# Kernel tuning notes

Hardware: AMD Instinct MI355X
Metric: run time of the kernel (lower is better)

Reference implementation:

```python
import jax, jax.numpy as jnp
import numpy as np

H = 3  # hidden size (matches nn.LSTM(3, 3, ...))


def _lstm_dir(x, Wih, Whh, bih, bhh, reverse):
    """One direction of one LSTM layer. x: [B,T,D]; PyTorch gate order i,f,g,o."""
    B = x.shape[0]
    xT = jnp.swapaxes(x, 0, 1)  # [T,B,D]
    # Precompute input projection for all timesteps (memory-bound GEMM once).
    x_proj = jnp.einsum('tbd,gd->tbg', xT, Wih) + (bih + bhh)  # [T,B,4H]

    def step(carry, xp):
        h, c = carry
        gates = xp + h @ Whh.T  # [B,4H]
        i = jax.nn.sigmoid(gates[:, :H])
        f = jax.nn.sigmoid(gates[:, H:2 * H])
        g = jnp.tanh(gates[:, 2 * H:3 * H])
        o = jax.nn.sigmoid(gates[:, 3 * H:])
        c = f * c + i * g
        h = o * jnp.tanh(c)
        return (h, c), h

    init = (jnp.zeros((B, H), x.dtype), jnp.zeros((B, H), x.dtype))
    _, hs = jax.lax.scan(step, init, x_proj, reverse=reverse)
    return jnp.swapaxes(hs, 0, 1)  # [B,T,H], time-aligned with input


def setup_inputs() -> dict:
    key = jax.random.key(0)
    ks = jax.random.split(key, 20)
    B, T = 8192, 512
    k = 1.0 / np.sqrt(H)

    def u(kk, shape):
        return jax.random.uniform(kk, shape, jnp.float32, -k, k)

    inp = {"x": jax.random.normal(ks[0], (B, T, 3), jnp.float32)}
    # layer 0: input dim 3; layer 1: input dim 2*H = 6
    inp.update({
        "W_ih_l0": u(ks[1], (4 * H, 3)),  "W_hh_l0": u(ks[2], (4 * H, H)),
        "b_ih_l0": u(ks[3], (4 * H,)),    "b_hh_l0": u(ks[4], (4 * H,)),
        "W_ih_l0r": u(ks[5], (4 * H, 3)), "W_hh_l0r": u(ks[6], (4 * H, H)),
        "b_ih_l0r": u(ks[7], (4 * H,)),   "b_hh_l0r": u(ks[8], (4 * H,)),
        "W_ih_l1": u(ks[9], (4 * H, 2 * H)),  "W_hh_l1": u(ks[10], (4 * H, H)),
        "b_ih_l1": u(ks[11], (4 * H,)),       "b_hh_l1": u(ks[12], (4 * H,)),
        "W_ih_l1r": u(ks[13], (4 * H, 2 * H)),"W_hh_l1r": u(ks[14], (4 * H, H)),
        "b_ih_l1r": u(ks[15], (4 * H,)),      "b_hh_l1r": u(ks[16], (4 * H,)),
        "W_lin": u(ks[17], (1, 2 * H)),       "b_lin": u(ks[18], (1,)),
    })
    return inp


def reference(x, W_ih_l0, W_hh_l0, b_ih_l0, b_hh_l0,
              W_ih_l0r, W_hh_l0r, b_ih_l0r, b_hh_l0r,
              W_ih_l1, W_hh_l1, b_ih_l1, b_hh_l1,
              W_ih_l1r, W_hh_l1r, b_ih_l1r, b_hh_l1r,
              W_lin, b_lin):
    # layer 0 (bidirectional)
    y0 = jnp.concatenate([
        _lstm_dir(x, W_ih_l0, W_hh_l0, b_ih_l0, b_hh_l0, False),
        _lstm_dir(x, W_ih_l0r, W_hh_l0r, b_ih_l0r, b_hh_l0r, True),
    ], axis=-1)  # [B,T,6]
    # layer 1 (bidirectional)
    y1 = jnp.concatenate([
        _lstm_dir(y0, W_ih_l1, W_hh_l1, b_ih_l1, b_hh_l1, False),
        _lstm_dir(y0, W_ih_l1r, W_hh_l1r, b_ih_l1r, b_hh_l1r, True),
    ], axis=-1)  # [B,T,6]
    last = y1[:, -1, :]  # [B,6]  (output sequence at final timestep)
    out = last @ W_lin.T + b_lin  # [B,1]
    return jax.nn.sigmoid(out.reshape(-1))  # [B]
```

## Files before the change

kernel.cpp:

```cpp
#include <hip/hip_runtime.h>


#define B_ 8192
#define T_ 512
#define LOG2E 1.4426950408889634f

typedef float v2f __attribute__((ext_vector_type(2)));

__device__ __forceinline__ float rcp_(float x)  { return __builtin_amdgcn_rcpf(x); }
__device__ __forceinline__ float exp2_(float x) { return __builtin_amdgcn_exp2f(x); }
__device__ __forceinline__ float sigm_(float x) {
  return rcp_(1.0f + exp2_(-LOG2E * x));
}
__device__ __forceinline__ float tanh_(float x) {
  return 1.0f - 2.0f * rcp_(1.0f + exp2_(2.0f * LOG2E * x));
}
__device__ __forceinline__ float act_(float p) { return rcp_(1.f + exp2_(p)); }

__device__ __forceinline__ v2f sp(float s) { return (v2f){s, s}; }
__device__ __forceinline__ v2f pkfma(v2f a, float b, v2f c) {
  return __builtin_elementwise_fma(a, sp(b), c);
}

#define PIN1(v) asm volatile("" : "+v"(v))
#define PIN2(v) do {                                                      \
    double _d = __builtin_bit_cast(double, v);                            \
    asm volatile("" : "+v"(_d));                                          \
    v = __builtin_bit_cast(v2f, _d); } while (0)

template <int CTRL>
__device__ __forceinline__ float dppf(float v) {
  int s = __float_as_int(v);
  return __int_as_float(__builtin_amdgcn_update_dpp(s, s, CTRL, 0xF, 0xF, false));
}
#define QP0 dppf<0x00>
#define QP1 dppf<0x55>
#define QP2 dppf<0xAA>
#define SHL4 0x104
#define SHR4 0x114

template <bool DIRB>
__device__ __forceinline__ void l0_run(
    const float* __restrict__ x,
    const float* __restrict__ Wi, const float* __restrict__ Wh,
    const float* __restrict__ bi, const float* __restrict__ bh,
    float* __restrict__ yout, int b, int jl)
{
  const int jj = (jl < 3) ? jl : 0;
  const int ri = jj, rf = 3 + jj, rg = 6 + jj, ro = 9 + jj;
  const float sL = -LOG2E, sG = -2.f * LOG2E;

  float wi_i0 = Wi[ri*3+0]*sL, wi_i1 = Wi[ri*3+1]*sL, wi_i2 = Wi[ri*3+2]*sL;
  float wi_f0 = Wi[rf*3+0]*sL, wi_f1 = Wi[rf*3+1]*sL, wi_f2 = Wi[rf*3+2]*sL;
  float wi_g0 = Wi[rg*3+0]*sG, wi_g1 = Wi[rg*3+1]*sG, wi_g2 = Wi[rg*3+2]*sG;
  float wi_o0 = Wi[ro*3+0]*sL, wi_o1 = Wi[ro*3+1]*sL, wi_o2 = Wi[ro*3+2]*sL;
  float wh_i0 = Wh[ri*3+0]*sL, wh_i1 = Wh[ri*3+1]*sL, wh_i2 = Wh[ri*3+2]*sL;
  float wh_f0 = Wh[rf*3+0]*sL, wh_f1 = Wh[rf*3+1]*sL, wh_f2 = Wh[rf*3+2]*sL;
  float wh_g0 = Wh[rg*3+0]*sG, wh_g1 = Wh[rg*3+1]*sG, wh_g2 = Wh[rg*3+2]*sG;
  float wh_o0 = Wh[ro*3+0]*sL, wh_o1 = Wh[ro*3+1]*sL, wh_o2 = Wh[ro*3+2]*sL;
  float b_i = (bi[ri]+bh[ri])*sL, b_f = (bi[rf]+bh[rf])*sL;
  float b_g = (bi[rg]+bh[rg])*sG, b_o = (bi[ro]+bh[ro])*sL;

  PIN1(wi_i0); PIN1(wi_i1); PIN1(wi_i2);
  PIN1(wi_f0); PIN1(wi_f1); PIN1(wi_f2);
  PIN1(wi_g0); PIN1(wi_g1); PIN1(wi_g2);
  PIN1(wi_o0); PIN1(wi_o1); PIN1(wi_o2);
  PIN1(wh_i0); PIN1(wh_i1); PIN1(wh_i2);
  PIN1(wh_f0); PIN1(wh_f1); PIN1(wh_f2);
  PIN1(wh_g0); PIN1(wh_g1); PIN1(wh_g2);
  PIN1(wh_o0); PIN1(wh_o1); PIN1(wh_o2);
  PIN1(b_i); PIN1(b_f); PIN1(b_g); PIN1(b_o);

  float h = 0.f, c = 0.f, ha0 = 0.f, ha1 = 0.f, ha2 = 0.f;
  float hs0, hs1, hs2, hs3, hs4, hs5, hs6, hs7;

  const float4* xq4 = (const float4*)(x + (size_t)b * (T_ * 3));
  float* ybase = yout + (size_t)b * (T_ * 3) + jj * 8;

  float4 p0, p1, p2, p3, p4, p5, q0, q1, q2, q3, q4, q5;

#define LDQ(blk, R0, R1, R2, R3, R4, R5) do {                             \
    const float4* _p = xq4 + (blk) * 6;                                   \
    R0 = _p[0]; R1 = _p[1]; R2 = _p[2];                                   \
    R3 = _p[3]; R4 = _p[4]; R5 = _p[5];                                   \
    __builtin_amdgcn_sched_barrier(0); } while (0)

#define STEPS(X0, X1, X2, HOUT) do {                                      \
    float _x0 = (X0), _x1 = (X1), _x2 = (X2);                             \
    float _pi = __builtin_fmaf(wi_i0, _x0, b_i);                          \
    _pi = __builtin_fmaf(wi_i1, _x1, _pi);                                \
    _pi = __builtin_fmaf(wi_i2, _x2, _pi);                                \
    float _qi = wh_i0 * ha0;                                              \
    _qi = __builtin_fmaf(wh_i1, ha1, _qi);                                \
    _qi = __builtin_fmaf(wh_i2, ha2, _qi);                                \
    float _pf = __builtin_fmaf(wi_f0, _x0, b_f);                          \
    _pf = __builtin_fmaf(wi_f1, _x1, _pf);                                \
    _pf = __builtin_fmaf(wi_f2, _x2, _pf);                                \
    float _qf = wh_f0 * ha0;                                              \
    _qf = __builtin_fmaf(wh_f1, ha1, _qf);                                \
    _qf = __builtin_fmaf(wh_f2, ha2, _qf);                                \
    float _pg = __builtin_fmaf(wi_g0, _x0, b_g);                          \
    _pg = __builtin_fmaf(wi_g1, _x1, _pg);                                \
    _pg = __builtin_fmaf(wi_g2, _x2, _pg);                                \
    float _qg = wh_g0 * ha0;                                              \
    _qg = __builtin_fmaf(wh_g1, ha1, _qg);                                \
    _qg = __builtin_fmaf(wh_g2, ha2, _qg);                                \
    float _po = __builtin_fmaf(wi_o0, _x0, b_o);                          \
    _po = __builtin_fmaf(wi_o1, _x1, _po);                                \
    _po = __builtin_fmaf(wi_o2, _x2, _po);                                \
    float _qo = wh_o0 * ha0;                                              \
    _qo = __builtin_fmaf(wh_o1, ha1, _qo);                                \
    _qo = __builtin_fmaf(wh_o2, ha2, _qo);                                \
    float _ig = act_(_pi + _qi);                                          \
    float _fg = act_(_pf + _qf);                                          \
    float _gg = __builtin_fmaf(2.f, act_(_pg + _qg), -1.f);               \
    float _og = act_(_po + _qo);                                          \
    c = __builtin_fmaf(_fg, c, _ig * _gg);                                \
    float _th = __builtin_fmaf(                                           \
        2.f, rcp_(1.f + exp2_(-2.f * LOG2E * c)), -1.f);                  \
    h = _og * _th;                                                        \
    ha0 = QP0(h); ha1 = QP1(h); ha2 = QP2(h);                             \
    HOUT = h; } while (0)

#define S0(R0,R1,R2,R3,R4,R5) STEPS(R0.x, R0.y, R0.z, hs0)
#define S1(R0,R1,R2,R3,R4,R5) STEPS(R0.w, R1.x, R1.y, hs1)
#define S2(R0,R1,R2,R3,R4,R5) STEPS(R1.z, R1.w, R2.x, hs2)
#define S3(R0,R1,R2,R3,R4,R5) STEPS(R2.y, R2.z, R2.w, hs3)
#define S4(R0,R1,R2,R3,R4,R5) STEPS(R3.x, R3.y, R3.z, hs4)
#define S5(R0,R1,R2,R3,R4,R5) STEPS(R3.w, R4.x, R4.y, hs5)
#define S6(R0,R1,R2,R3,R4,R5) STEPS(R4.z, R4.w, R5.x, hs6)
#define S7(R0,R1,R2,R3,R4,R5) STEPS(R5.y, R5.z, R5.w, hs7)

#define PROCQ(R0,R1,R2,R3,R4,R5) do {                                     \
    if (DIRB) {                                                           \
      S7(R0,R1,R2,R3,R4,R5); S6(R0,R1,R2,R3,R4,R5);                       \
      S5(R0,R1,R2,R3,R4,R5); S4(R0,R1,R2,R3,R4,R5);                       \
      S3(R0,R1,R2,R3,R4,R5); S2(R0,R1,R2,R3,R4,R5);                       \
      S1(R0,R1,R2,R3,R4,R5); S0(R0,R1,R2,R3,R4,R5);                       \
    } else {                                                              \
      S0(R0,R1,R2,R3,R4,R5); S1(R0,R1,R2,R3,R4,R5);                       \
      S2(R0,R1,R2,R3,R4,R5); S3(R0,R1,R2,R3,R4,R5);                       \
      S4(R0,R1,R2,R3,R4,R5); S5(R0,R1,R2,R3,R4,R5);                       \
      S6(R0,R1,R2,R3,R4,R5); S7(R0,R1,R2,R3,R4,R5);                       \
    } } while (0)

#define STQ(blk) do {                                                     \
    if (jl < 3) {                                                         \
      float4* _o = (float4*)(ybase + (blk) * 24);                         \
      _o[0] = make_float4(hs0, hs1, hs2, hs3);                            \
      _o[1] = make_float4(hs4, hs5, hs6, hs7);                            \
    } } while (0)

#define BLK(k) (DIRB ? (63 - (k)) : (k))

  LDQ(BLK(0), p0, p1, p2, p3, p4, p5);
  LDQ(BLK(1), q0, q1, q2, q3, q4, q5);
  for (int k = 0; k < 64; k += 2) {
    PROCQ(p0, p1, p2, p3, p4, p5);
    STQ(BLK(k));
    if (k + 2 < 64) LDQ(BLK(k + 2), p0, p1, p2, p3, p4, p5);
    PROCQ(q0, q1, q2, q3, q4, q5);
    STQ(BLK(k + 1));
    if (k + 3 < 64) LDQ(BLK(k + 3), q0, q1, q2, q3, q4, q5);
  }
#undef LDQ
#undef STEPS
#undef S0
#undef S1
#undef S2
#undef S3
#undef S4
#undef S5
#undef S6
#undef S7
#undef PROCQ
#undef STQ
#undef BLK
}

__global__ __launch_bounds__(256) void lstm_l0_scalar(
    const float* __restrict__ x,
    const float* __restrict__ Wf_ih, const float* __restrict__ Wf_hh,
    const float* __restrict__ bf_ih, const float* __restrict__ bf_hh,
    const float* __restrict__ Wr_ih, const float* __restrict__ Wr_hh,
    const float* __restrict__ br_ih, const float* __restrict__ br_hh,
    float* __restrict__ y0f, float* __restrict__ y0b)
{
  int gid = blockIdx.x * 256 + threadIdx.x;
  const int nfwd = B_ * 4;
  if (gid < nfwd) {
    int b = gid >> 2, jl = gid & 3;
    l0_run<false>(x, Wf_ih, Wf_hh, bf_ih, bf_hh, y0f, b, jl);
  } else {
    int g2 = gid - nfwd;
    int b = g2 >> 2, jl = g2 & 3;
    l0_run<true>(x, Wr_ih, Wr_hh, br_ih, br_hh, y0b, b, jl);
  }
}

#define CELL_TAIL(HOUT)                                                   \
    float r0v = act_(pv.x);                                               \
    float ayv = act_(pv.y);                                               \
    float axv = __builtin_fmaf(avx, r0v, dvx);                            \
    float slx = dppf<SHL4>(axv), sly = dppf<SHL4>(ayv);                   \
    float srx = dppf<SHR4>(axv), sry = dppf<SHR4>(ayv);                   \
    float pig = axv * (qgo ? srx : slx);                                  \
    float gf  = qgo ? sry : ayv;                                          \
    float gO  = qgo ? ayv : sly;                                          \
    c = __builtin_fmaf(gf, c, pig);                                       \
    float th = __builtin_fmaf(                                            \
        2.f, rcp_(1.f + exp2_(-2.f * LOG2E * c)), -1.f);                  \
    h = gO * th;                                                          \
    ha0 = QP0(h); ha1 = QP1(h); ha2 = QP2(h);                             \
    HOUT = h;

__global__ __launch_bounds__(256) void lstm_l1_fwd(
    const float* __restrict__ Wih1, const float* __restrict__ Whh1,
    const float* __restrict__ bih1, const float* __restrict__ bhh1,
    const float* __restrict__ Wih1r,
    const float* __restrict__ bih1r, const float* __restrict__ bhh1r,
    const float* __restrict__ Wlin, const float* __restrict__ blin,
    const float* __restrict__ y0f, const float* __restrict__ y0b,
    float* __restrict__ out)
{
  int tid  = blockIdx.x * 256 + threadIdx.x;
  int b    = tid >> 3;
  int lane = tid & 7;
  bool qgo = (lane & 4) != 0;
  int j = lane & 3; int jj = (j < 3) ? j : 0;
  const int ra = (qgo ? 6 : 0) + jj, rb = ra + 3;
  const float kx = qgo ? (-2.f * LOG2E) : (-LOG2E);
  const float ky = -LOG2E;
  const float avx = qgo ? 2.f : 1.f;
  const float dvx = qgo ? -1.f : 0.f;

  v2f w0 = {Wih1[ra*6+0]*kx, Wih1[rb*6+0]*ky},
      w1 = {Wih1[ra*6+1]*kx, Wih1[rb*6+1]*ky},
      w2 = {Wih1[ra*6+2]*kx, Wih1[rb*6+2]*ky},
      w3 = {Wih1[ra*6+3]*kx, Wih1[rb*6+3]*ky},
      w4 = {Wih1[ra*6+4]*kx, Wih1[rb*6+4]*ky},
      w5 = {Wih1[ra*6+5]*kx, Wih1[rb*6+5]*ky};
  v2f u0 = {Whh1[ra*3+0]*kx, Whh1[rb*3+0]*ky},
      u1 = {Whh1[ra*3+1]*kx, Whh1[rb*3+1]*ky},
      u2 = {Whh1[ra*3+2]*kx, Whh1[rb*3+2]*ky};
  v2f b2 = {(bih1[ra]+bhh1[ra])*kx, (bih1[rb]+bhh1[rb])*ky};
  PIN2(w0); PIN2(w1); PIN2(w2); PIN2(w3); PIN2(w4); PIN2(w5);
  PIN2(u0); PIN2(u1); PIN2(u2); PIN2(b2);

  const float4* yfq = (const float4*)(y0f + (size_t)b * (T_ * 3));
  const float4* ybq = (const float4*)(y0b + (size_t)b * (T_ * 3));

  const float* ufp = y0f + (size_t)b * (T_ * 3) + 63 * 24 + 7;
  const float* ubp = y0b + (size_t)b * (T_ * 3) + 63 * 24 + 7;

  float h = 0.f, c = 0.f, ha0 = 0.f, ha1 = 0.f, ha2 = 0.f;
  float hs0, hs1, hs2, hs3, hs4, hs5, hs6, hs7;
  float4 pf0, pf1, pf2, pf3, pf4, pf5, pb0, pb1, pb2, pb3, pb4, pb5;
  float4 qf0, qf1, qf2, qf3, qf4, qf5, qb0, qb1, qb2, qb3, qb4, qb5;

#define LDB(blk, F0,F1,F2,F3,F4,F5, G0,G1,G2,G3,G4,G5) do {               \
    const float4* _f = yfq + (blk) * 6;                                   \
    const float4* _g = ybq + (blk) * 6;                                   \
    F0 = _f[0]; F1 = _f[1]; F2 = _f[2];                                   \
    F3 = _f[3]; F4 = _f[4]; F5 = _f[5];                                   \
    G0 = _g[0]; G1 = _g[1]; G2 = _g[2];                                   \
    G3 = _g[3]; G4 = _g[4]; G5 = _g[5];                                   \
    __builtin_amdgcn_sched_barrier(0); } while (0)

#define STEPB(f0, f1, f2, g0, g1, g2, HOUT) do {                          \
    v2f pv = pkfma(w0, (f0), b2); pv = pkfma(w1, (f1), pv);               \
    pv = pkfma(w2, (f2), pv);                                             \
    v2f nv = w3 * sp(g0); nv = pkfma(w4, (g1), nv);                       \
    nv = pkfma(w5, (g2), nv);                                             \
    v2f uv = u0 * sp(ha0); uv = pkfma(u1, ha1, uv);                       \
    uv = pkfma(u2, ha2, uv);                                              \
    pv = (pv + nv) + uv;                                                  \
    CELL_TAIL(HOUT) } while (0)

#define PROCB(F0,F1,F2,F3,F4,F5, G0,G1,G2,G3,G4,G5) do {                  \
    STEPB(F0.x, F2.x, F4.x,  G0.x, G2.x, G4.x, hs0);                      \
    STEPB(F0.y, F2.y, F4.y,  G0.y, G2.y, G4.y, hs1);                      \
    STEPB(F0.z, F2.z, F4.z,  G0.z, G2.z, G4.z, hs2);                      \
    STEPB(F0.w, F2.w, F4.w,  G0.w, G2.w, G4.w, hs3);                      \
    STEPB(F1.x, F3.x, F5.x,  G1.x, G3.x, G5.x, hs4);                      \
    STEPB(F1.y, F3.y, F5.y,  G1.y, G3.y, G5.y, hs5);                      \
    STEPB(F1.z, F3.z, F5.z,  G1.z, G3.z, G5.z, hs6);                      \
    STEPB(F1.w, F3.w, F5.w,  G1.w, G3.w, G5.w, hs7); } while (0)

  LDB(0, pf0,pf1,pf2,pf3,pf4,pf5, pb0,pb1,pb2,pb3,pb4,pb5);
  LDB(1, qf0,qf1,qf2,qf3,qf4,qf5, qb0,qb1,qb2,qb3,qb4,qb5);
  for (int it = 0; it < 32; ++it) {
    PROCB(pf0,pf1,pf2,pf3,pf4,pf5, pb0,pb1,pb2,pb3,pb4,pb5);
    if (it < 31) LDB(2*it+2, pf0,pf1,pf2,pf3,pf4,pf5, pb0,pb1,pb2,pb3,pb4,pb5);
    PROCB(qf0,qf1,qf2,qf3,qf4,qf5, qb0,qb1,qb2,qb3,qb4,qb5);
    if (it < 31) LDB(2*it+3, qf0,qf1,qf2,qf3,qf4,qf5, qb0,qb1,qb2,qb3,qb4,qb5);
  }
  (void)hs0; (void)hs1; (void)hs2; (void)hs3;
  (void)hs4; (void)hs5; (void)hs6; (void)hs7;

  float uf0 = ufp[0], uf1 = ufp[8], uf2 = ufp[16];
  float ub0 = ubp[0], ub1 = ubp[8], ub2 = ubp[16];

  float h1b;
  {
    v2f r0 = {Wih1r[ra*6+0]*kx, Wih1r[rb*6+0]*ky},
        r1 = {Wih1r[ra*6+1]*kx, Wih1r[rb*6+1]*ky},
        r2 = {Wih1r[ra*6+2]*kx, Wih1r[rb*6+2]*ky},
        r3 = {Wih1r[ra*6+3]*kx, Wih1r[rb*6+3]*ky},
        r4 = {Wih1r[ra*6+4]*kx, Wih1r[rb*6+4]*ky},
        r5 = {Wih1r[ra*6+5]*kx, Wih1r[rb*6+5]*ky};
    v2f br = {(bih1r[ra]+bhh1r[ra])*kx, (bih1r[rb]+bhh1r[rb])*ky};
    v2f qv = pkfma(r0, uf0, br); qv = pkfma(r1, uf1, qv);
    qv = pkfma(r2, uf2, qv);     qv = pkfma(r3, ub0, qv);
    qv = pkfma(r4, ub1, qv);     qv = pkfma(r5, ub2, qv);
    float r0v = act_(qv.x);
    float ayv = act_(qv.y);
    float axv = __builtin_fmaf(avx, r0v, dvx);
    float slx = dppf<SHL4>(axv), sly = dppf<SHL4>(ayv);
    float srx = dppf<SHR4>(axv);
    float gi = qgo ? srx : axv;
    float gG = qgo ? axv : slx;
    float gO = qgo ? ayv : sly;
    float cb = gi * gG;
    h1b = gO * tanh_(cb);
  }

  float part = 0.f;
  if (!qgo && j < 3) part = __builtin_fmaf(Wlin[j], h, Wlin[3 + j] * h1b);
  part += __shfl_xor(part, 1, 8);
  part += __shfl_xor(part, 2, 8);
  part += __shfl_xor(part, 4, 8);
  if (lane == 0) out[b] = sigm_(part + blin[0]);
#undef LDB
#undef STEPB
#undef PROCB
}

extern "C" void kernel_launch(void* const* d_in, const int* in_sizes, int n_in,
                              void* d_out, int out_size, void* d_ws, size_t ws_size,
                              hipStream_t stream) {
  const float* x        = (const float*)d_in[0];
  const float* W_ih_l0  = (const float*)d_in[1];
  const float* W_hh_l0  = (const float*)d_in[2];
  const float* b_ih_l0  = (const float*)d_in[3];
  const float* b_hh_l0  = (const float*)d_in[4];
  const float* W_ih_l0r = (const float*)d_in[5];
  const float* W_hh_l0r = (const float*)d_in[6];
  const float* b_ih_l0r = (const float*)d_in[7];
  const float* b_hh_l0r = (const float*)d_in[8];
  const float* W_ih_l1  = (const float*)d_in[9];
  const float* W_hh_l1  = (const float*)d_in[10];
  const float* b_ih_l1  = (const float*)d_in[11];
  const float* b_hh_l1  = (const float*)d_in[12];
  const float* W_ih_l1r = (const float*)d_in[13];
  const float* b_ih_l1r = (const float*)d_in[15];
  const float* b_hh_l1r = (const float*)d_in[16];
  const float* W_lin    = (const float*)d_in[17];
  const float* b_lin    = (const float*)d_in[18];

  float* y0f = (float*)d_ws;
  float* y0b = (float*)d_ws + (size_t)B_ * T_ * 3;
  float* out = (float*)d_out;

  lstm_l0_scalar<<<(B_ * 4 * 2) / 256, 256, 0, stream>>>(
      x, W_ih_l0, W_hh_l0, b_ih_l0, b_hh_l0,
      W_ih_l0r, W_hh_l0r, b_ih_l0r, b_hh_l0r, y0f, y0b);

  lstm_l1_fwd<<<(B_ * 8) / 256, 256, 0, stream>>>(
      W_ih_l1, W_hh_l1, b_ih_l1, b_hh_l1,
      W_ih_l1r, b_ih_l1r, b_hh_l1r,
      W_lin, b_lin, y0f, y0b, out);
}
```

Before: 145.9 us.

## Split layer-0 LSTM gates across 8 lanes per batch with packed FMA

Layer 0 now uses 8 lanes per (batch, direction) instead of 4. Each lane computes two gate pre-activations as a packed v2f, with the (i,f) pair on one half of the lanes and the (g,o) pair on the other. Gate values are exchanged between the halves using DPP row shifts. This cuts the serial per-step dependency chain per thread but doubles the thread count, and launch bounds now request 2 blocks. The cost is more waves, duplicated loads of x, and extra DPP traffic.

After: 166.9 us. 14.4% more time.

```diff
diff --git a/kernel.cpp b/kernel.cpp
--- a/kernel.cpp
+++ b/kernel.cpp
@@ -22,7 +22,6 @@
   return __builtin_elementwise_fma(a, sp(b), c);
 }
 
-#define PIN1(v) asm volatile("" : "+v"(v))
 #define PIN2(v) do {                                                      \
     double _d = __builtin_bit_cast(double, v);                            \
     asm volatile("" : "+v"(_d));                                          \
@@ -40,98 +39,73 @@
 #define SHR4 0x114
 
 template <bool DIRB>
-__device__ __forceinline__ void l0_run(
+__device__ __forceinline__ void l0_dir(
     const float* __restrict__ x,
     const float* __restrict__ Wi, const float* __restrict__ Wh,
     const float* __restrict__ bi, const float* __restrict__ bh,
-    float* __restrict__ yout, int b, int jl)
+    float* __restrict__ yout, int b, int lane)
 {
-  const int jj = (jl < 3) ? jl : 0;
-  const int ri = jj, rf = 3 + jj, rg = 6 + jj, ro = 9 + jj;
-  const float sL = -LOG2E, sG = -2.f * LOG2E;
-
-  float wi_i0 = Wi[ri*3+0]*sL, wi_i1 = Wi[ri*3+1]*sL, wi_i2 = Wi[ri*3+2]*sL;
-  float wi_f0 = Wi[rf*3+0]*sL, wi_f1 = Wi[rf*3+1]*sL, wi_f2 = Wi[rf*3+2]*sL;
-  float wi_g0 = Wi[rg*3+0]*sG, wi_g1 = Wi[rg*3+1]*sG, wi_g2 = Wi[rg*3+2]*sG;
-  float wi_o0 = Wi[ro*3+0]*sL, wi_o1 = Wi[ro*3+1]*sL, wi_o2 = Wi[ro*3+2]*sL;
-  float wh_i0 = Wh[ri*3+0]*sL, wh_i1 = Wh[ri*3+1]*sL, wh_i2 = Wh[ri*3+2]*sL;
-  float wh_f0 = Wh[rf*3+0]*sL, wh_f1 = Wh[rf*3+1]*sL, wh_f2 = Wh[rf*3+2]*sL;
-  float wh_g0 = Wh[rg*3+0]*sG, wh_g1 = Wh[rg*3+1]*sG, wh_g2 = Wh[rg*3+2]*sG;
-  float wh_o0 = Wh[ro*3+0]*sL, wh_o1 = Wh[ro*3+1]*sL, wh_o2 = Wh[ro*3+2]*sL;
-  float b_i = (bi[ri]+bh[ri])*sL, b_f = (bi[rf]+bh[rf])*sL;
-  float b_g = (bi[rg]+bh[rg])*sG, b_o = (bi[ro]+bh[ro])*sL;
-
-  PIN1(wi_i0); PIN1(wi_i1); PIN1(wi_i2);
-  PIN1(wi_f0); PIN1(wi_f1); PIN1(wi_f2);
-  PIN1(wi_g0); PIN1(wi_g1); PIN1(wi_g2);
-  PIN1(wi_o0); PIN1(wi_o1); PIN1(wi_o2);
-  PIN1(wh_i0); PIN1(wh_i1); PIN1(wh_i2);
-  PIN1(wh_f0); PIN1(wh_f1); PIN1(wh_f2);
-  PIN1(wh_g0); PIN1(wh_g1); PIN1(wh_g2);
-  PIN1(wh_o0); PIN1(wh_o1); PIN1(wh_o2);
-  PIN1(b_i); PIN1(b_f); PIN1(b_g); PIN1(b_o);
+  bool qgo = (lane & 4) != 0;
+  int j = lane & 3; int jj = (j < 3) ? j : 0;
+  const int ra = (qgo ? 6 : 0) + jj, rb = ra + 3;
+  const float kx = qgo ? (-2.f * LOG2E) : (-LOG2E);
+  const float ky = -LOG2E;
+  const float avx = qgo ? 2.f : 1.f;
+  const float dvx = qgo ? -1.f : 0.f;
+
+  v2f w0 = {Wi[ra*3+0]*kx, Wi[rb*3+0]*ky},
+      w1 = {Wi[ra*3+1]*kx, Wi[rb*3+1]*ky},
+      w2 = {Wi[ra*3+2]*kx, Wi[rb*3+2]*ky};
+  v2f u0 = {Wh[ra*3+0]*kx, Wh[rb*3+0]*ky},
+      u1 = {Wh[ra*3+1]*kx, Wh[rb*3+1]*ky},
+      u2 = {Wh[ra*3+2]*kx, Wh[rb*3+2]*ky};
+  v2f b2 = {(bi[ra]+bh[ra])*kx, (bi[rb]+bh[rb])*ky};
 
   float h = 0.f, c = 0.f, ha0 = 0.f, ha1 = 0.f, ha2 = 0.f;
   float hs0, hs1, hs2, hs3, hs4, hs5, hs6, hs7;
 
-  const float4* xq4 = (const float4*)(x + (size_t)b * (T_ * 3));
-  float* ybase = yout + (size_t)b * (T_ * 3) + jj * 8;
+  const float4* xq = (const float4*)(x + (size_t)b * (T_ * 3));
+  float* ywb = yout + (size_t)b * (T_ * 3) + jj * 8;
 
   float4 p0, p1, p2, p3, p4, p5, q0, q1, q2, q3, q4, q5;
 
-#define LDQ(blk, R0, R1, R2, R3, R4, R5) do {                             \
-    const float4* _p = xq4 + (blk) * 6;                                   \
+#define LD1(blk, R0, R1, R2, R3, R4, R5) do {                             \
+    const float4* _p = xq + (blk) * 6;                                    \
     R0 = _p[0]; R1 = _p[1]; R2 = _p[2];                                   \
     R3 = _p[3]; R4 = _p[4]; R5 = _p[5];                                   \
     __builtin_amdgcn_sched_barrier(0); } while (0)
 
-#define STEPS(X0, X1, X2, HOUT) do {                                      \
-    float _x0 = (X0), _x1 = (X1), _x2 = (X2);                             \
-    float _pi = __builtin_fmaf(wi_i0, _x0, b_i);                          \
-    _pi = __builtin_fmaf(wi_i1, _x1, _pi);                                \
-    _pi = __builtin_fmaf(wi_i2, _x2, _pi);                                \
-    float _qi = wh_i0 * ha0;                                              \
-    _qi = __builtin_fmaf(wh_i1, ha1, _qi);                                \
-    _qi = __builtin_fmaf(wh_i2, ha2, _qi);                                \
-    float _pf = __builtin_fmaf(wi_f0, _x0, b_f);                          \
-    _pf = __builtin_fmaf(wi_f1, _x1, _pf);                                \
-    _pf = __builtin_fmaf(wi_f2, _x2, _pf);                                \
-    float _qf = wh_f0 * ha0;                                              \
-    _qf = __builtin_fmaf(wh_f1, ha1, _qf);                                \
-    _qf = __builtin_fmaf(wh_f2, ha2, _qf);                                \
-    float _pg = __builtin_fmaf(wi_g0, _x0, b_g);                          \
-    _pg = __builtin_fmaf(wi_g1, _x1, _pg);                                \
-    _pg = __builtin_fmaf(wi_g2, _x2, _pg);                                \
-    float _qg = wh_g0 * ha0;                                              \
-    _qg = __builtin_fmaf(wh_g1, ha1, _qg);                                \
-    _qg = __builtin_fmaf(wh_g2, ha2, _qg);                                \
-    float _po = __builtin_fmaf(wi_o0, _x0, b_o);                          \
-    _po = __builtin_fmaf(wi_o1, _x1, _po);                                \
-    _po = __builtin_fmaf(wi_o2, _x2, _po);                                \
-    float _qo = wh_o0 * ha0;                                              \
-    _qo = __builtin_fmaf(wh_o1, ha1, _qo);                                \
-    _qo = __builtin_fmaf(wh_o2, ha2, _qo);                                \
-    float _ig = act_(_pi + _qi);                                          \
-    float _fg = act_(_pf + _qf);                                          \
-    float _gg = __builtin_fmaf(2.f, act_(_pg + _qg), -1.f);               \
-    float _og = act_(_po + _qo);                                          \
-    c = __builtin_fmaf(_fg, c, _ig * _gg);                                \
-    float _th = __builtin_fmaf(                                           \
+#define STEP1(x0, x1, x2, HOUT) do {                                      \
+    v2f pv = pkfma(w0, (x0), b2); pv = pkfma(w1, (x1), pv);               \
+    pv = pkfma(w2, (x2), pv);                                             \
+    v2f uv = u0 * sp(ha0); uv = pkfma(u1, ha1, uv);                       \
+    uv = pkfma(u2, ha2, uv);                                              \
+    pv = pv + uv;                                                         \
+    float r0v = act_(pv.x);                                               \
+    float ayv = act_(pv.y);                         \
+    float axv = __builtin_fmaf(avx, r0v, dvx);  \
+    float slx = dppf<SHL4>(axv), sly = dppf<SHL4>(ayv);                   \
+    float srx = dppf<SHR4>(axv), sry = dppf<SHR4>(ayv);                   \
+    float pig = axv * (qgo ? srx : slx);           \
+    float gf  = qgo ? sry : ayv;                                          \
+    float gO  = qgo ? ayv : sly;                                          \
+    c = __builtin_fmaf(gf, c, pig);                                       \
+    float th = __builtin_fmaf(                                            \
         2.f, rcp_(1.f + exp2_(-2.f * LOG2E * c)), -1.f);                  \
-    h = _og * _th;                                                        \
+    h = gO * th;                                                          \
     ha0 = QP0(h); ha1 = QP1(h); ha2 = QP2(h);                             \
     HOUT = h; } while (0)
 
-#define S0(R0,R1,R2,R3,R4,R5) STEPS(R0.x, R0.y, R0.z, hs0)
-#define S1(R0,R1,R2,R3,R4,R5) STEPS(R0.w, R1.x, R1.y, hs1)
-#define S2(R0,R1,R2,R3,R4,R5) STEPS(R1.z, R1.w, R2.x, hs2)
-#define S3(R0,R1,R2,R3,R4,R5) STEPS(R2.y, R2.z, R2.w, hs3)
-#define S4(R0,R1,R2,R3,R4,R5) STEPS(R3.x, R3.y, R3.z, hs4)
-#define S5(R0,R1,R2,R3,R4,R5) STEPS(R3.w, R4.x, R4.y, hs5)
-#define S6(R0,R1,R2,R3,R4,R5) STEPS(R4.z, R4.w, R5.x, hs6)
-#define S7(R0,R1,R2,R3,R4,R5) STEPS(R5.y, R5.z, R5.w, hs7)
-
-#define PROCQ(R0,R1,R2,R3,R4,R5) do {                                     \
+#define S0(R0,R1,R2,R3,R4,R5) STEP1(R0.x, R0.y, R0.z, hs0)
+#define S1(R0,R1,R2,R3,R4,R5) STEP1(R0.w, R1.x, R1.y, hs1)
+#define S2(R0,R1,R2,R3,R4,R5) STEP1(R1.z, R1.w, R2.x, hs2)
+#define S3(R0,R1,R2,R3,R4,R5) STEP1(R2.y, R2.z, R2.w, hs3)
+#define S4(R0,R1,R2,R3,R4,R5) STEP1(R3.x, R3.y, R3.z, hs4)
+#define S5(R0,R1,R2,R3,R4,R5) STEP1(R3.w, R4.x, R4.y, hs5)
+#define S6(R0,R1,R2,R3,R4,R5) STEP1(R4.z, R4.w, R5.x, hs6)
+#define S7(R0,R1,R2,R3,R4,R5) STEP1(R5.y, R5.z, R5.w, hs7)
+
+#define PROC1(R0,R1,R2,R3,R4,R5) do {                                     \
     if (DIRB) {                                                           \
       S7(R0,R1,R2,R3,R4,R5); S6(R0,R1,R2,R3,R4,R5);                       \
       S5(R0,R1,R2,R3,R4,R5); S4(R0,R1,R2,R3,R4,R5);                       \
@@ -144,27 +118,27 @@
       S6(R0,R1,R2,R3,R4,R5); S7(R0,R1,R2,R3,R4,R5);                       \
     } } while (0)
 
-#define STQ(blk) do {                                                     \
-    if (jl < 3) {                                                         \
-      float4* _o = (float4*)(ybase + (blk) * 24);                         \
+#define FLUSH1(blk) do {                                                  \
+    if (lane < 3) {                                                       \
+      float4* _o = (float4*)(ywb + (blk) * 24);                           \
       _o[0] = make_float4(hs0, hs1, hs2, hs3);                            \
       _o[1] = make_float4(hs4, hs5, hs6, hs7);                            \
     } } while (0)
 
 #define BLK(k) (DIRB ? (63 - (k)) : (k))
 
-  LDQ(BLK(0), p0, p1, p2, p3, p4, p5);
-  LDQ(BLK(1), q0, q1, q2, q3, q4, q5);
+  LD1(BLK(0), p0, p1, p2, p3, p4, p5);
+  LD1(BLK(1), q0, q1, q2, q3, q4, q5);
   for (int k = 0; k < 64; k += 2) {
-    PROCQ(p0, p1, p2, p3, p4, p5);
-    STQ(BLK(k));
-    if (k + 2 < 64) LDQ(BLK(k + 2), p0, p1, p2, p3, p4, p5);
-    PROCQ(q0, q1, q2, q3, q4, q5);
-    STQ(BLK(k + 1));
-    if (k + 3 < 64) LDQ(BLK(k + 3), q0, q1, q2, q3, q4, q5);
+    PROC1(p0, p1, p2, p3, p4, p5);
+    FLUSH1(BLK(k));
+    if (k + 2 < 64) LD1(BLK(k + 2), p0, p1, p2, p3, p4, p5);
+    PROC1(q0, q1, q2, q3, q4, q5);
+    FLUSH1(BLK(k + 1));
+    if (k + 3 < 64) LD1(BLK(k + 3), q0, q1, q2, q3, q4, q5);
   }
-#undef LDQ
-#undef STEPS
+#undef LD1
+#undef STEP1
 #undef S0
 #undef S1
 #undef S2
@@ -173,12 +147,12 @@
 #undef S5
 #undef S6
 #undef S7
-#undef PROCQ
-#undef STQ
+#undef PROC1
+#undef FLUSH1
 #undef BLK
 }
 
-__global__ __launch_bounds__(256) void lstm_l0_scalar(
+__global__ __launch_bounds__(256, 2) void lstm_l0_pair(
     const float* __restrict__ x,
     const float* __restrict__ Wf_ih, const float* __restrict__ Wf_hh,
     const float* __restrict__ bf_ih, const float* __restrict__ bf_hh,
@@ -187,14 +161,12 @@
     float* __restrict__ y0f, float* __restrict__ y0b)
 {
   int gid = blockIdx.x * 256 + threadIdx.x;
-  const int nfwd = B_ * 4;
+  const int nfwd = B_ * 8;
   if (gid < nfwd) {
-    int b = gid >> 2, jl = gid & 3;
-    l0_run<false>(x, Wf_ih, Wf_hh, bf_ih, bf_hh, y0f, b, jl);
+    l0_dir<false>(x, Wf_ih, Wf_hh, bf_ih, bf_hh, y0f, gid >> 3, gid & 7);
   } else {
     int g2 = gid - nfwd;
-    int b = g2 >> 2, jl = g2 & 3;
-    l0_run<true>(x, Wr_ih, Wr_hh, br_ih, br_hh, y0b, b, jl);
+    l0_dir<true>(x, Wr_ih, Wr_hh, br_ih, br_hh, y0b, g2 >> 3, g2 & 7);
   }
 }
 
@@ -362,7 +334,7 @@
   float* y0b = (float*)d_ws + (size_t)B_ * T_ * 3;
   float* out = (float*)d_out;
 
-  lstm_l0_scalar<<<(B_ * 4 * 2) / 256, 256, 0, stream>>>(
+  lstm_l0_pair<<<(B_ * 8 * 2) / 256, 256, 0, stream>>>(
       x, W_ih_l0, W_hh_l0, b_ih_l0, b_hh_l0,
       W_ih_l0r, W_hh_l0r, b_ih_l0r, b_hh_l0r, y0f, y0b);
 
```
